# Performance work log

Hardware: AMD Instinct MI355X
Metric: run time of the kernel (lower is better)

## Reference

```python
import jax, jax.numpy as jnp
import numpy as np

B, H, S, D = 2, 16, 2048, 128
NEG = -1.0e9  # matches masked_fill_(-1000000000.0)


def setup_inputs() -> dict:
    key = jax.random.key(0)
    kq, kk, kv = jax.random.split(key, 3)
    Q = jax.random.normal(kq, (B, H, S, D), dtype=jnp.float32)
    K = jax.random.normal(kk, (B, H, S, D), dtype=jnp.float32)
    V = jax.random.normal(kv, (B, H, S, D), dtype=jnp.float32)
    # causal mask: True means masked (filled with -1e9)
    causal = jnp.triu(jnp.ones((S, S), dtype=jnp.bool_), k=1)
    attn_mask = jnp.broadcast_to(causal, (B, H, S, S))
    return {"Q": Q, "K": K, "V": V, "attn_mask": attn_mask}


def reference(Q, K, V, attn_mask):
    d_k = K.shape[-1]
    scale = 1.0 / np.sqrt(d_k).astype(np.float32)
    # [B,H,S,S]
    scores = jnp.einsum('bhqd,bhkd->bhqk', Q, K) * scale
    scores = jnp.where(attn_mask, NEG, scores)
    attn = jax.nn.softmax(scores, axis=-1)
    # dropout p=0.0 -> identity
    context = jnp.einsum('bhqk,bhkd->bhqd', attn, V)
    return context
```

## Files before the change

### kernel.cpp

```cpp
#include <hip/hip_runtime.h>
#include <hip/hip_bf16.h>


#define S_LEN 2048
#define D_DIM 128
#define KTILE 64
#define QSCALE 0.12751743f

typedef __attribute__((ext_vector_type(8))) short short8;
typedef __attribute__((ext_vector_type(4))) short short4v;
typedef __attribute__((ext_vector_type(4))) float float4v;

#define KROW 136
#define VROW 72
#define PROW 72
#define KS_OFF 0
#define VT_OFF 8704
#define PS_OFF 17920
#define LDS_SHORTS 22528

static __device__ __forceinline__ short f2bs(float f) {
    union { __hip_bfloat16 h; short s; } u;
    u.h = __float2bfloat16(f);
    return u.s;
}

__global__ __launch_bounds__(256, 2)
void sdpa_causal_kernel(const float* __restrict__ Qg,
                        const float* __restrict__ Kg,
                        const float* __restrict__ Vg,
                        float* __restrict__ Og) {
    __shared__ __align__(16) short lds[LDS_SHORTS];
    short* Ks = lds + KS_OFF;
    short* Vt = lds + VT_OFF;
    short* Ps = lds + PS_OFF;

    const int t    = threadIdx.x;
    const int w    = t >> 6;
    const int l    = t & 63;
    const int lc   = l & 15;
    const int quad = l >> 4;

    const int id  = blockIdx.x;
    const int a   = id >> 3;
    const int bh  = ((id & 7) << 2) + (a >> 4);
    const int prr = a & 15;
    const int pr  = (a & 32) ? (15 - prr) : prr;
    const int qtA = 31 - pr;
    const int qtB = pr;

    const size_t base = (size_t)bh * S_LEN * D_DIM;

    const int q0A = qtA * 64 + w * 16;
    const int q0B = qtB * 64 + w * 16;

    short8 qaA[4], qaB[4];
    {
        const float* qpA = Qg + base + (size_t)(q0A + lc) * D_DIM;
        const float* qpB = Qg + base + (size_t)(q0B + lc) * D_DIM;
        for (int kc = 0; kc < 4; ++kc) {
            const float4* pA = (const float4*)(qpA + kc * 32 + quad * 8);
            const float4* pB = (const float4*)(qpB + kc * 32 + quad * 8);
            float4 a0 = pA[0], a1 = pA[1], b0 = pB[0], b1 = pB[1];
            short8 fA, fB;
            fA[0]=f2bs(a0.x*QSCALE); fA[1]=f2bs(a0.y*QSCALE);
            fA[2]=f2bs(a0.z*QSCALE); fA[3]=f2bs(a0.w*QSCALE);
            fA[4]=f2bs(a1.x*QSCALE); fA[5]=f2bs(a1.y*QSCALE);
            fA[6]=f2bs(a1.z*QSCALE); fA[7]=f2bs(a1.w*QSCALE);
            fB[0]=f2bs(b0.x*QSCALE); fB[1]=f2bs(b0.y*QSCALE);
            fB[2]=f2bs(b0.z*QSCALE); fB[3]=f2bs(b0.w*QSCALE);
            fB[4]=f2bs(b1.x*QSCALE); fB[5]=f2bs(b1.y*QSCALE);
            fB[6]=f2bs(b1.z*QSCALE); fB[7]=f2bs(b1.w*QSCALE);
            qaA[kc] = fA; qaB[kc] = fB;
        }
    }

    float4v oA[8], oB[8];
    for (int n = 0; n < 8; ++n) {
        oA[n] = (float4v){0.f,0.f,0.f,0.f};
        oB[n] = (float4v){0.f,0.f,0.f,0.f};
    }
    float lsA[4] = {0.f,0.f,0.f,0.f};
    float lsB[4] = {0.f,0.f,0.f,0.f};

    const int kk_t = t >> 5;
    const int kd_t = (t & 31) << 2;
    const int vk_t = t & 63;
    const int vd_t = (t >> 6) << 3;

    const int ntiles = qtA + 1;

    float4 kreg[8], vreg[8];
    for (int g = 0; g < 8; ++g) {
        kreg[g] = *(const float4*)(Kg + base + (size_t)(kk_t + 8*g) * D_DIM + kd_t);
        vreg[g] = *(const float4*)(Vg + base + (size_t)vk_t * D_DIM + 4*(vd_t + g));
    }

    auto computeTile = [&](const short8* qa, float4v* o, float* ls,
                           int q0, int kb, bool straddle) {
        float4v sf[4];
        for (int n = 0; n < 4; ++n) {
            const short* kr = &Ks[(n * 16 + lc) * KROW];
            float4v s = (float4v){0.f,0.f,0.f,0.f};
            for (int kc = 0; kc < 4; ++kc)
                s = __builtin_amdgcn_mfma_f32_16x16x32_bf16(
                        qa[kc], *(const short8*)&kr[kc * 32 + quad * 8], s, 0, 0, 0);
            sf[n] = s;
        }
        if (straddle) {
            for (int n = 0; n < 4; ++n) {
                const int key = kb + n * 16 + lc;
                for (int r = 0; r < 4; ++r)
                    if (key > q0 + quad * 4 + r) sf[n][r] = -INFINITY;
            }
        }
        for (int n = 0; n < 4; ++n)
            for (int r = 0; r < 4; ++r) {
                const float p = exp2f(sf[n][r]);
                sf[n][r] = p;
                ls[r] += p;
            }
        short* Pw = Ps + w * 16 * PROW;
        for (int n = 0; n < 4; ++n)
            for (int r = 0; r < 4; ++r)
                Pw[(quad * 4 + r) * PROW + n * 16 + lc] = f2bs(sf[n][r]);
        __asm__ volatile("" ::: "memory");
        short8 pa0 = *(const short8*)&Pw[lc * PROW + quad * 8];
        short8 pa1 = *(const short8*)&Pw[lc * PROW + 32 + quad * 8];
        for (int nd = 0; nd < 8; ++nd) {
            const short* vr = &Vt[(nd * 16 + lc) * VROW];
            o[nd] = __builtin_amdgcn_mfma_f32_16x16x32_bf16(
                        pa0, *(const short8*)&vr[quad * 8], o[nd], 0, 0, 0);
            o[nd] = __builtin_amdgcn_mfma_f32_16x16x32_bf16(
                        pa1, *(const short8*)&vr[32 + quad * 8], o[nd], 0, 0, 0);
        }
    };

    for (int kt = 0; kt < ntiles; ++kt) {
        const int kb = kt * KTILE;

        __syncthreads();

        for (int g = 0; g < 8; ++g) {
            short4v ks = { f2bs(kreg[g].x), f2bs(kreg[g].y),
                           f2bs(kreg[g].z), f2bs(kreg[g].w) };
            *(short4v*)&Ks[(kk_t + 8*g) * KROW + kd_t] = ks;
            const int vd = 4 * (vd_t + g);
            Vt[(vd + 0) * VROW + vk_t] = f2bs(vreg[g].x);
            Vt[(vd + 1) * VROW + vk_t] = f2bs(vreg[g].y);
            Vt[(vd + 2) * VROW + vk_t] = f2bs(vreg[g].z);
            Vt[(vd + 3) * VROW + vk_t] = f2bs(vreg[g].w);
        }

        if (kt + 1 < ntiles) {
            const size_t koff = base + (size_t)(kt + 1) * KTILE * D_DIM;
            for (int g = 0; g < 8; ++g) {
                kreg[g] = *(const float4*)(Kg + koff + (size_t)(kk_t + 8*g) * D_DIM + kd_t);
                vreg[g] = *(const float4*)(Vg + koff + (size_t)vk_t * D_DIM + 4*(vd_t + g));
            }
        }

        __syncthreads();

        computeTile(qaA, oA, lsA, q0A, kb, kt == qtA);
        if (kt <= qtB)
            computeTile(qaB, oB, lsB, q0B, kb, kt == qtB);
    }

    auto storeO = [&](const float4v* o, const float* ls, int q0) {
        float inv[4];
        for (int r = 0; r < 4; ++r) {
            float s = ls[r];
            for (int mask = 1; mask < 16; mask <<= 1)
                s += __shfl_xor(s, mask);
            inv[r] = 1.0f / s;
        }
        const size_t ob = base + (size_t)q0 * D_DIM;
        for (int nd = 0; nd < 8; ++nd)
            for (int r = 0; r < 4; ++r)
                Og[ob + (size_t)(quad * 4 + r) * D_DIM + nd * 16 + lc] = o[nd][r] * inv[r];
    };
    storeO(oA, lsA, q0A);
    storeO(oB, lsB, q0B);
}

extern "C" void kernel_launch(void* const* d_in, const int* in_sizes, int n_in,
                              void* d_out, int out_size, void* d_ws, size_t ws_size,
                              hipStream_t stream) {
    (void)in_sizes; (void)n_in; (void)d_ws; (void)ws_size; (void)out_size;
    const float* Qg = (const float*)d_in[0];
    const float* Kg = (const float*)d_in[1];
    const float* Vg = (const float*)d_in[2];
    float* Og = (float*)d_out;
    sdpa_causal_kernel<<<dim3(512), dim3(256), 0, stream>>>(Qg, Kg, Vg, Og);
}
```

Before: 723.1 us.

## Pair adjacent query tiles per block and share K/V fragment loads across both

```diff
diff --git a/kernel.cpp b/kernel.cpp
--- a/kernel.cpp
+++ b/kernel.cpp
@@ -17,7 +17,7 @@
 #define KS_OFF 0
 #define VT_OFF 8704
 #define PS_OFF 17920
-#define LDS_SHORTS 22528
+#define LDS_SHORTS 27136
 
 static __device__ __forceinline__ short f2bs(float f) {
     union { __hip_bfloat16 h; short s; } u;
@@ -46,8 +46,8 @@
     const int bh  = ((id & 7) << 2) + (a >> 4);
     const int prr = a & 15;
     const int pr  = (a & 32) ? (15 - prr) : prr;
-    const int qtA = 31 - pr;
-    const int qtB = pr;
+    const int qtA = 2 * pr + 1;
+    const int qtB = 2 * pr;
 
     const size_t base = (size_t)bh * S_LEN * D_DIM;
 
@@ -96,45 +96,7 @@
         vreg[g] = *(const float4*)(Vg + base + (size_t)vk_t * D_DIM + 4*(vd_t + g));
     }
 
-    auto computeTile = [&](const short8* qa, float4v* o, float* ls,
-                           int q0, int kb, bool straddle) {
-        float4v sf[4];
-        for (int n = 0; n < 4; ++n) {
-            const short* kr = &Ks[(n * 16 + lc) * KROW];
-            float4v s = (float4v){0.f,0.f,0.f,0.f};
-            for (int kc = 0; kc < 4; ++kc)
-                s = __builtin_amdgcn_mfma_f32_16x16x32_bf16(
-                        qa[kc], *(const short8*)&kr[kc * 32 + quad * 8], s, 0, 0, 0);
-            sf[n] = s;
-        }
-        if (straddle) {
-            for (int n = 0; n < 4; ++n) {
-                const int key = kb + n * 16 + lc;
-                for (int r = 0; r < 4; ++r)
-                    if (key > q0 + quad * 4 + r) sf[n][r] = -INFINITY;
-            }
-        }
-        for (int n = 0; n < 4; ++n)
-            for (int r = 0; r < 4; ++r) {
-                const float p = exp2f(sf[n][r]);
-                sf[n][r] = p;
-                ls[r] += p;
-            }
-        short* Pw = Ps + w * 16 * PROW;
-        for (int n = 0; n < 4; ++n)
-            for (int r = 0; r < 4; ++r)
-                Pw[(quad * 4 + r) * PROW + n * 16 + lc] = f2bs(sf[n][r]);
-        __asm__ volatile("" ::: "memory");
-        short8 pa0 = *(const short8*)&Pw[lc * PROW + quad * 8];
-        short8 pa1 = *(const short8*)&Pw[lc * PROW + 32 + quad * 8];
-        for (int nd = 0; nd < 8; ++nd) {
-            const short* vr = &Vt[(nd * 16 + lc) * VROW];
-            o[nd] = __builtin_amdgcn_mfma_f32_16x16x32_bf16(
-                        pa0, *(const short8*)&vr[quad * 8], o[nd], 0, 0, 0);
-            o[nd] = __builtin_amdgcn_mfma_f32_16x16x32_bf16(
-                        pa1, *(const short8*)&vr[32 + quad * 8], o[nd], 0, 0, 0);
-        }
-    };
+    short* Pw = Ps + w * 32 * PROW;
 
     for (int kt = 0; kt < ntiles; ++kt) {
         const int kb = kt * KTILE;
@@ -162,9 +124,62 @@
 
         __syncthreads();
 
-        computeTile(qaA, oA, lsA, q0A, kb, kt == qtA);
-        if (kt <= qtB)
-            computeTile(qaB, oB, lsB, q0B, kb, kt == qtB);
+        const bool bAct = (kt <= qtB);
+        const bool strA = (kt == qtA);
+        const bool strB = (kt == qtB);
+
+        for (int n = 0; n < 4; ++n) {
+            const short* kr = &Ks[(n * 16 + lc) * KROW];
+            float4v sA = (float4v){0.f,0.f,0.f,0.f};
+            float4v sB = (float4v){0.f,0.f,0.f,0.f};
+            for (int kc = 0; kc < 4; ++kc) {
+                const short8 kf = *(const short8*)&kr[kc * 32 + quad * 8];
+                sA = __builtin_amdgcn_mfma_f32_16x16x32_bf16(qaA[kc], kf, sA, 0, 0, 0);
+                if (bAct)
+                    sB = __builtin_amdgcn_mfma_f32_16x16x32_bf16(qaB[kc], kf, sB, 0, 0, 0);
+            }
+            const int key = kb + n * 16 + lc;
+            if (strA) {
+                for (int r = 0; r < 4; ++r)
+                    if (key > q0A + quad * 4 + r) sA[r] = -INFINITY;
+            }
+            for (int r = 0; r < 4; ++r) {
+                const float p = exp2f(sA[r]);
+                lsA[r] += p;
+                Pw[(quad * 4 + r) * PROW + n * 16 + lc] = f2bs(p);
+            }
+            if (bAct) {
+                if (strB) {
+                    for (int r = 0; r < 4; ++r)
+                        if (key > q0B + quad * 4 + r) sB[r] = -INFINITY;
+                }
+                for (int r = 0; r < 4; ++r) {
+                    const float p = exp2f(sB[r]);
+                    lsB[r] += p;
+                    Pw[(16 + quad * 4 + r) * PROW + n * 16 + lc] = f2bs(p);
+                }
+            }
+        }
+        __asm__ volatile("" ::: "memory");
+
+        const short8 pa0A = *(const short8*)&Pw[lc * PROW + quad * 8];
+        const short8 pa1A = *(const short8*)&Pw[lc * PROW + 32 + quad * 8];
+        short8 pa0B = pa0A, pa1B = pa1A;
+        if (bAct) {
+            pa0B = *(const short8*)&Pw[(16 + lc) * PROW + quad * 8];
+            pa1B = *(const short8*)&Pw[(16 + lc) * PROW + 32 + quad * 8];
+        }
+        for (int nd = 0; nd < 8; ++nd) {
+            const short* vr = &Vt[(nd * 16 + lc) * VROW];
+            const short8 v0 = *(const short8*)&vr[quad * 8];
+            const short8 v1 = *(const short8*)&vr[32 + quad * 8];
+            oA[nd] = __builtin_amdgcn_mfma_f32_16x16x32_bf16(pa0A, v0, oA[nd], 0, 0, 0);
+            oA[nd] = __builtin_amdgcn_mfma_f32_16x16x32_bf16(pa1A, v1, oA[nd], 0, 0, 0);
+            if (bAct) {
+                oB[nd] = __builtin_amdgcn_mfma_f32_16x16x32_bf16(pa0B, v0, oB[nd], 0, 0, 0);
+                oB[nd] = __builtin_amdgcn_mfma_f32_16x16x32_bf16(pa1B, v1, oB[nd], 0, 0, 0);
+            }
+        }
     }
 
     auto storeO = [&](const float4v* o, const float* ls, int q0) {
```

Result: slower. 747.4 us (+3.4%).
